# Kernel optimization log

Measured on AMD Instinct MI355X. Metric: run time of the kernel, lower is better.

## Reference

```python
import jax, jax.numpy as jnp
import numpy as np

NUM_HEADS = 16
ROPE_THETA = 10000.0


def _vision_rope_tables(seq_len, head_dim):
    # Llama4 vision ('mllama4') 2D rotary: x/y patch-grid positions,
    # interleaved (non-neox) complex pairs. Returns cos/sin [S, head_dim//2].
    idx = int(np.sqrt(seq_len))  # patches per side (24 for 336/14)
    pos = np.arange(seq_len)
    fx = (pos % idx + 1).astype(np.float32)
    fy = (pos // idx + 1).astype(np.float32)
    freq_dim = head_dim // 2
    rope_freq = 1.0 / ROPE_THETA ** (
        np.arange(0, freq_dim, 2)[: freq_dim // 2].astype(np.float32) / freq_dim
    )
    fx = np.repeat(fx[:, None] * rope_freq[None, :], 2, axis=-1)  # [S, freq_dim]
    fy = np.repeat(fy[:, None] * rope_freq[None, :], 2, axis=-1)
    freqs = np.concatenate([fx, fy], axis=-1)[:, ::2]  # [S, head_dim//2]
    return jnp.asarray(np.cos(freqs)), jnp.asarray(np.sin(freqs))


def _apply_rope(x, cos, sin):
    # x: [B, S, H, D]; even/odd interleaved pairs treated as complex numbers
    B, S, H, D = x.shape
    xr = x.reshape(B, S, H, D // 2, 2)
    x0, x1 = xr[..., 0], xr[..., 1]
    c = cos[None, :, None, :]
    s = sin[None, :, None, :]
    o0 = x0 * c - x1 * s
    o1 = x0 * s + x1 * c
    return jnp.stack([o0, o1], axis=-1).reshape(B, S, H, D)


def setup_inputs() -> dict:
    key = jax.random.key(0)
    ks = jax.random.split(key, 5)
    E = 1408
    B, S = 16, 576
    scale = 0.02
    return {
        "hidden_states": jax.random.normal(ks[0], (B, S, E), dtype=jnp.float32),
        "w_qkv": jax.random.normal(ks[1], (E, 3 * E), dtype=jnp.float32) * scale,
        "b_qkv": jax.random.normal(ks[2], (3 * E,), dtype=jnp.float32) * scale,
        "w_o": jax.random.normal(ks[3], (E, E), dtype=jnp.float32) * scale,
        "b_o": jax.random.normal(ks[4], (E,), dtype=jnp.float32) * scale,
    }


def reference(hidden_states, w_qkv, b_qkv, w_o, b_o):
    B, S, E = hidden_states.shape
    H = NUM_HEADS
    D = E // H
    scaling = D ** -0.5

    qkv = hidden_states @ w_qkv + b_qkv  # [B,S,3E]
    q, k, v = jnp.split(qkv, 3, axis=-1)
    q = q.reshape(B, S, H, D)
    k = k.reshape(B, S, H, D)
    v = v.reshape(B, S, H, D)

    cos, sin = _vision_rope_tables(S, D)
    q = _apply_rope(q, cos, sin)
    k = _apply_rope(k, cos, sin)

    q = q * scaling
    scores = jnp.einsum("bqhd,bkhd->bhqk", q, k)  # full bidirectional attention
    probs = jax.nn.softmax(scores, axis=-1)
    attn = jnp.einsum("bhqk,bkhd->bqhd", probs, v).reshape(B, S, E)

    return attn @ w_o + b_o
```

## Files before the change

### kernel.cpp

```cpp
#include <hip/hip_runtime.h>
#include <hip/hip_bf16.h>


typedef unsigned short UST;
typedef __attribute__((ext_vector_type(8))) __bf16 bf16x8;
typedef __attribute__((ext_vector_type(4))) float f32x4;
typedef __attribute__((ext_vector_type(8))) UST us8;
typedef __attribute__((ext_vector_type(4))) UST us4;

typedef __attribute__((address_space(3))) unsigned int lds_u32;
typedef const __attribute__((address_space(1))) unsigned int glob_u32;

static __device__ __forceinline__ float bf2f(UST u){
  unsigned int x = ((unsigned int)u) << 16;
  return __builtin_bit_cast(float, x);
}
static __device__ __forceinline__ UST f2bf(float f){
  unsigned int x = __builtin_bit_cast(unsigned int, f);
  x += 0x7fffu + ((x >> 16) & 1u);
  return (UST)(x >> 16);
}

__global__ void k_tables(float* __restrict__ cosT, float* __restrict__ sinT){
  int s = blockIdx.x;
  int d = threadIdx.x;
  if (d >= 88) return;
  int p = d >> 1;
  int tt = p % 22;
  double comp = (p < 22) ? (double)(s % 24 + 1) : (double)(s / 24 + 1);
  double a = comp * pow(10000.0, -(double)tt / 22.0);
  cosT[d*576 + s] = (float)cos(a);
  sinT[d*576 + s] = (float)sin(a);
}

__global__ void k_zero(UST* __restrict__ qa, UST* __restrict__ ka, UST* __restrict__ vt){
  int c = blockIdx.x*256 + threadIdx.x;
  int bh = c / 576, s = c - bh*576;
  us8 z = {0,0,0,0,0,0,0,0};
  *(us8*)(qa + ((size_t)bh*576 + s)*96 + 88) = z;
  *(us8*)(ka + ((size_t)bh*576 + s)*96 + 88) = z;
  *(us8*)(vt + (size_t)bh*55296 + 50688 + s*8) = z;
}

__global__ void k_cvt(const float* __restrict__ in, UST* __restrict__ out, int n4){
  int i = blockIdx.x * 256 + threadIdx.x;
  if (i >= n4) return;
  float4 v = ((const float4*)in)[i];
  us4 o; o[0]=f2bf(v.x); o[1]=f2bf(v.y); o[2]=f2bf(v.z); o[3]=f2bf(v.w);
  *(us4*)(out + 4*(size_t)i) = o;
}

__global__ void k_cvt_t(const float* __restrict__ W, UST* __restrict__ Bt, int K, int N){
  __shared__ __align__(16) UST tl[64][70];
  int kt = blockIdx.x, nt = blockIdx.y;
  int t = threadIdx.x;
  int k = t >> 2, u = t & 3;
  const float* src = W + (size_t)(kt*64 + k)*N + nt*64 + u*16;
#pragma unroll
  for (int i = 0; i < 4; ++i){
    float4 v = *(const float4*)(src + 4*i);
    UST* d = &tl[k][u*16 + 4*i];
    d[0]=f2bf(v.x); d[1]=f2bf(v.y); d[2]=f2bf(v.z); d[3]=f2bf(v.w);
  }
  __syncthreads();
  int n = t >> 2;
  UST* dst = Bt + (size_t)(nt*64 + n)*K + kt*64 + u*16;
#pragma unroll
  for (int i = 0; i < 2; ++i){
    us8 o;
#pragma unroll
    for (int j = 0; j < 8; ++j) o[j] = tl[u*16 + 8*i + j][n];
    *(us8*)(dst + 8*i) = o;
  }
}

template<int EPI>
__global__ __launch_bounds__(256, 2) void k_gemm(
    const UST* __restrict__ A, const UST* __restrict__ Bt,
    const float* __restrict__ bias, void* __restrict__ Cout,
    int M, int N, int K,
    UST* __restrict__ qa, UST* __restrict__ ka, UST* __restrict__ vt,
    const float* __restrict__ cosT, const float* __restrict__ sinT)
{
  __shared__ __align__(16) UST lA[2][128][64];
  __shared__ __align__(16) UST lB[2][128][64];
  const int t = threadIdx.x;
  const int bm = blockIdx.x, bn = blockIdx.y;
  const int wave = t >> 6, lane = t & 63;
  const int lm = lane & 15, g = lane >> 4;
  const int wr = (wave >> 1) << 6, wc = (wave & 1) << 6;
  const int lrow = lane >> 3;
  const int lcol = (((lane & 7) ^ lrow) << 3);
  const UST* Ag = A  + (size_t)(bm*128 + wave*32 + lrow)*K + lcol;
  const UST* Bg = Bt + (size_t)(bn*128 + wave*32 + lrow)*K + lcol;

  f32x4 zero = {0.f,0.f,0.f,0.f};
  f32x4 acc[4][4];
#pragma unroll
  for (int i=0;i<4;++i)
#pragma unroll
    for (int j=0;j<4;++j) acc[i][j] = zero;

  const int nkt = K >> 6;
  auto stage = [&](int kt, int buf){
#pragma unroll
    for (int c = 0; c < 4; ++c){
      __builtin_amdgcn_global_load_lds((glob_u32*)(Ag + (size_t)kt*64 + (size_t)(8*c)*K),
                                       (lds_u32*)(&lA[buf][wave*32 + 8*c][0]), 16, 0, 0);
      __builtin_amdgcn_global_load_lds((glob_u32*)(Bg + (size_t)kt*64 + (size_t)(8*c)*K),
                                       (lds_u32*)(&lB[buf][wave*32 + 8*c][0]), 16, 0, 0);
    }
  };

  stage(0, 0);
  __syncthreads();
  const int swz = (lm & 7) << 3;

  for (int kt = 0; kt < nkt; ++kt){
    const int cur = kt & 1;
    if (kt + 1 < nkt) stage(kt + 1, cur ^ 1);
#pragma unroll
    for (int ks = 0; ks < 2; ++ks){
      bf16x8 af[4], bfv[4];
      const int cb = (ks*32 + g*8) ^ swz;
#pragma unroll
      for (int mf = 0; mf < 4; ++mf)
        af[mf] = __builtin_bit_cast(bf16x8, *(const us8*)&lA[cur][wr + mf*16 + lm][cb]);
#pragma unroll
      for (int nf = 0; nf < 4; ++nf)
        bfv[nf] = __builtin_bit_cast(bf16x8, *(const us8*)&lB[cur][wc + nf*16 + lm][cb]);
#pragma unroll
      for (int mf = 0; mf < 4; ++mf)
#pragma unroll
        for (int nf = 0; nf < 4; ++nf)
          acc[mf][nf] = __builtin_amdgcn_mfma_f32_16x16x32_bf16(af[mf], bfv[nf], acc[mf][nf], 0, 0, 0);
    }
    __syncthreads();
  }

  if (EPI == 0){
#pragma unroll
    for (int nf = 0; nf < 4; ++nf){
      const int col = bn*128 + wc + nf*16 + lm;
      const float bv = bias[col];
#pragma unroll
      for (int mf = 0; mf < 4; ++mf){
        const size_t rb = (size_t)(bm*128 + wr + mf*16 + g*4);
#pragma unroll
        for (int r = 0; r < 4; ++r)
          ((float*)Cout)[(rb + r)*(size_t)N + col] = acc[mf][nf][r] + bv;
      }
    }
  } else {
    const int j = bn / 11;
    const int bnr = bn - j*11;
    if (j == 2){
#pragma unroll
      for (int nf = 0; nf < 4; ++nf){
        const int cv = bnr*128 + wc + nf*16 + lm;
        const float bv = bias[2816 + cv];
        const int h = cv / 88, d = cv - h*88;
#pragma unroll
        for (int mf = 0; mf < 4; ++mf){
          const int rb = bm*128 + wr + mf*16 + g*4;
          const int b2 = rb / 576, s = rb - b2*576;
          UST* dst = vt + ((size_t)((b2*16 + h)*96 + d))*576 + s;
          us4 pk;
#pragma unroll
          for (int r = 0; r < 4; ++r) pk[r] = f2bf(acc[mf][nf][r] + bv);
          *(us4*)dst = pk;
        }
      }
    } else {
      UST* outp = j ? ka : qa;
      const float sc = j ? 1.0f : 0.10660035817780521f;
      const bool even = (lm & 1) == 0;
#pragma unroll
      for (int nf = 0; nf < 4; ++nf){
        const int cv = bnr*128 + wc + nf*16 + lm;
        const float bv = bias[j*1408 + cv];
        const int h = cv / 88, d = cv - h*88;
        const float* cT = cosT + d*576;
        const float* sT = sinT + d*576;
#pragma unroll
        for (int mf = 0; mf < 4; ++mf){
          const int rb = bm*128 + wr + mf*16 + g*4;
          const int b2 = rb / 576, s = rb - b2*576;
          float4 c4 = *(const float4*)(cT + s);
          float4 s4 = *(const float4*)(sT + s);
          float cc[4] = {c4.x, c4.y, c4.z, c4.w};
          float ss[4] = {s4.x, s4.y, s4.z, s4.w};
          UST* dst = outp + ((size_t)(b2*16 + h)*576 + s)*96 + d;
#pragma unroll
          for (int r = 0; r < 4; ++r){
            float vs = acc[mf][nf][r] + bv;
            float vo = __shfl_xor(vs, 1, 64);
            float o = even ? (vs*cc[r] - vo*ss[r])
                           : (vo*ss[r] + vs*cc[r]);
            dst[(size_t)r*96] = f2bf(o * sc);
          }
        }
      }
    }
  }
}

__global__ __launch_bounds__(256, 2) void k_attn(
    const UST* __restrict__ qa, const UST* __restrict__ ka,
    const UST* __restrict__ vt, UST* __restrict__ outp)
{
  __shared__ __align__(16) UST lK[64][104];
  __shared__ __align__(16) UST lV[96][72];
  __shared__ __align__(16) UST lP[4][16][72];
  const int bh = blockIdx.x, qt = blockIdx.y;
  const int t = threadIdx.x, wave = t >> 6, lane = t & 63;
  const int lm = lane & 15, g = lane >> 4;
  const int h = bh & 15, b = bh >> 4;

  bf16x8 qf[3];
  {
    const UST* qp = qa + ((size_t)bh*576 + qt*64 + wave*16 + lm)*96 + g*8;
#pragma unroll
    for (int ks = 0; ks < 3; ++ks) qf[ks] = __builtin_bit_cast(bf16x8, *(const us8*)(qp + ks*32));
  }
  f32x4 zero = {0.f,0.f,0.f,0.f};
  f32x4 acc[6];
#pragma unroll
  for (int i = 0; i < 6; ++i) acc[i] = zero;
  float mrun[4], lrun[4];
#pragma unroll
  for (int r = 0; r < 4; ++r){ mrun[r] = -1e30f; lrun[r] = 0.f; }

  const UST* kbase = ka + (size_t)bh*576*96;
  const UST* vbase = vt + (size_t)bh*96*576;

  for (int kvt = 0; kvt < 9; ++kvt){
    {
      int r = t >> 2, u = t & 3;
      const UST* src = kbase + (size_t)(kvt*64 + r)*96 + u*24;
#pragma unroll
      for (int i = 0; i < 3; ++i)
        *(uint4*)&lK[r][u*24 + i*8] = *(const uint4*)(src + i*8);
    }
    if (t < 192){
      int d = t >> 1, hf = t & 1;
      const UST* src = vbase + (size_t)d*576 + kvt*64 + hf*32;
#pragma unroll
      for (int i = 0; i < 4; ++i)
        *(uint4*)&lV[d][hf*32 + i*8] = *(const uint4*)(src + i*8);
    }
    __syncthreads();

    f32x4 sc[4];
#pragma unroll
    for (int i = 0; i < 4; ++i) sc[i] = zero;
#pragma unroll
    for (int ks = 0; ks < 3; ++ks){
#pragma unroll
      for (int nf = 0; nf < 4; ++nf){
        bf16x8 kf = __builtin_bit_cast(bf16x8, *(const us8*)&lK[nf*16 + lm][ks*32 + g*8]);
        sc[nf] = __builtin_amdgcn_mfma_f32_16x16x32_bf16(qf[ks], kf, sc[nf], 0, 0, 0);
      }
    }
    float mx[4];
#pragma unroll
    for (int r = 0; r < 4; ++r)
      mx[r] = fmaxf(fmaxf(sc[0][r], sc[1][r]), fmaxf(sc[2][r], sc[3][r]));
#pragma unroll
    for (int m = 1; m <= 8; m <<= 1)
#pragma unroll
      for (int r = 0; r < 4; ++r) mx[r] = fmaxf(mx[r], __shfl_xor(mx[r], m, 64));
    float al[4];
#pragma unroll
    for (int r = 0; r < 4; ++r){
      float mnew = fmaxf(mrun[r], mx[r]);
      float corr = __expf(mrun[r] - mnew);
      mrun[r] = mnew;
      lrun[r] *= corr;
      float ls = 0.f;
#pragma unroll
      for (int nf = 0; nf < 4; ++nf){
        float p = __expf(sc[nf][r] - mnew);
        sc[nf][r] = p;
        ls += p;
      }
#pragma unroll
      for (int df = 0; df < 6; ++df) acc[df][r] *= corr;
      al[r] = ls;
    }
#pragma unroll
    for (int m = 1; m <= 8; m <<= 1)
#pragma unroll
      for (int r = 0; r < 4; ++r) al[r] += __shfl_xor(al[r], m, 64);
#pragma unroll
    for (int r = 0; r < 4; ++r) lrun[r] += al[r];

#pragma unroll
    for (int nf = 0; nf < 4; ++nf)
#pragma unroll
      for (int r = 0; r < 4; ++r)
        lP[wave][4*g + r][nf*16 + lm] = f2bf(sc[nf][r]);

    bf16x8 pa[2];
#pragma unroll
    for (int ks2 = 0; ks2 < 2; ++ks2)
      pa[ks2] = __builtin_bit_cast(bf16x8, *(const us8*)&lP[wave][lm][ks2*32 + g*8]);
#pragma unroll
    for (int ks2 = 0; ks2 < 2; ++ks2)
#pragma unroll
      for (int df = 0; df < 6; ++df){
        bf16x8 vf = __builtin_bit_cast(bf16x8, *(const us8*)&lV[df*16 + lm][ks2*32 + g*8]);
        acc[df] = __builtin_amdgcn_mfma_f32_16x16x32_bf16(pa[ks2], vf, acc[df], 0, 0, 0);
      }
    __syncthreads();
  }

  float inv[4];
#pragma unroll
  for (int r = 0; r < 4; ++r) inv[r] = 1.f / lrun[r];
  const size_t rowt = (size_t)b*576 + qt*64 + wave*16;
#pragma unroll
  for (int df = 0; df < 6; ++df){
    int d = df*16 + lm;
    if (d < 88){
#pragma unroll
      for (int r = 0; r < 4; ++r)
        outp[(rowt + 4*g + r)*1408 + h*88 + d] = f2bf(acc[df][r] * inv[r]);
    }
  }
}

extern "C" void kernel_launch(void* const* d_in, const int* in_sizes, int n_in,
                              void* d_out, int out_size, void* d_ws, size_t ws_size,
                              hipStream_t stream)
{
  (void)in_sizes; (void)n_in; (void)out_size; (void)ws_size;
  const float* hs   = (const float*)d_in[0];
  const float* wqkv = (const float*)d_in[1];
  const float* bqkv = (const float*)d_in[2];
  const float* wo   = (const float*)d_in[3];
  const float* bo   = (const float*)d_in[4];
  float* out = (float*)d_out;

  char* w = (char*)d_ws;
  UST* A_bf   = (UST*)(w);
  UST* Bt1    = (UST*)(w + 25952256);
  UST* Bt2    = (UST*)(w + 37847040);
  UST* qa     = (UST*)(w + 41811968);
  UST* ka     = (UST*)(w + 70123520);
  UST* vt     = (UST*)(w + 98435072);
  float* cosT = (float*)(w + 126746624);
  float* sinT = (float*)(w + 126949376);

  k_tables<<<576, 128, 0, stream>>>(cosT, sinT);
  k_zero<<<576, 256, 0, stream>>>(qa, ka, vt);
  k_cvt<<<12672, 256, 0, stream>>>(hs, A_bf, 3244032);
  k_cvt_t<<<dim3(22, 66), 256, 0, stream>>>(wqkv, Bt1, 1408, 4224);
  k_cvt_t<<<dim3(22, 22), 256, 0, stream>>>(wo, Bt2, 1408, 1408);
  k_gemm<3><<<dim3(72, 33), 256, 0, stream>>>(A_bf, Bt1, bqkv, nullptr, 9216, 4224, 1408,
                                              qa, ka, vt, cosT, sinT);
  k_attn<<<dim3(256, 9), 256, 0, stream>>>(qa, ka, vt, A_bf);
  k_gemm<0><<<dim3(72, 11), 256, 0, stream>>>(A_bf, Bt2, bo, out, 9216, 1408, 1408,
                                              nullptr, nullptr, nullptr, nullptr, nullptr);
}
```

Baseline: 330.0 us.

## Process two query tiles per attention block and pack RoPE epilogue stores

The attention kernel now handles two 64-row query tiles per block, so each loaded K/V tile in LDS serves 128 queries and block count drops from 9 to 5 per head. The last block handles one tile. Separately, the QKV GEMM RoPE epilogue has lane pairs each write two adjacent bf16 outputs as one 32-bit store, and loads only the two cos/sin values it needs. This trades more registers (two accumulator sets) and fewer blocks, with some load imbalance, for halved K/V global traffic and fewer narrow stores.

```diff
diff --git a/kernel.cpp b/kernel.cpp
--- a/kernel.cpp
+++ b/kernel.cpp
@@ -175,29 +175,38 @@
       UST* outp = j ? ka : qa;
       const float sc = j ? 1.0f : 0.10660035817780521f;
       const bool even = (lm & 1) == 0;
+      const int r0 = (lm & 1) * 2;
 #pragma unroll
       for (int nf = 0; nf < 4; ++nf){
         const int cv = bnr*128 + wc + nf*16 + lm;
         const float bv = bias[j*1408 + cv];
         const int h = cv / 88, d = cv - h*88;
+        const int de = d & ~1;
         const float* cT = cosT + d*576;
         const float* sT = sinT + d*576;
 #pragma unroll
         for (int mf = 0; mf < 4; ++mf){
           const int rb = bm*128 + wr + mf*16 + g*4;
           const int b2 = rb / 576, s = rb - b2*576;
-          float4 c4 = *(const float4*)(cT + s);
-          float4 s4 = *(const float4*)(sT + s);
-          float cc[4] = {c4.x, c4.y, c4.z, c4.w};
-          float ss[4] = {s4.x, s4.y, s4.z, s4.w};
-          UST* dst = outp + ((size_t)(b2*16 + h)*576 + s)*96 + d;
+          float2 c2 = *(const float2*)(cT + s + r0);
+          float2 s2 = *(const float2*)(sT + s + r0);
+          UST* dstE = outp + ((size_t)(b2*16 + h)*576 + s)*96 + de;
+          float vs[4], vo[4];
 #pragma unroll
           for (int r = 0; r < 4; ++r){
-            float vs = acc[mf][nf][r] + bv;
-            float vo = __shfl_xor(vs, 1, 64);
-            float o = even ? (vs*cc[r] - vo*ss[r])
-                           : (vo*ss[r] + vs*cc[r]);
-            dst[(size_t)r*96] = f2bf(o * sc);
+            vs[r] = acc[mf][nf][r] + bv;
+            vo[r] = __shfl_xor(vs[r], 1, 64);
+          }
+          float cc[2] = {c2.x, c2.y}, ss[2] = {s2.x, s2.y};
+#pragma unroll
+          for (int rr = 0; rr < 2; ++rr){
+            const int r = r0 + rr;
+            float x0 = even ? vs[r] : vo[r];
+            float x1 = even ? vo[r] : vs[r];
+            float o0 = (x0*cc[rr] - x1*ss[rr])*sc;
+            float o1 = (x0*ss[rr] + x1*cc[rr])*sc;
+            unsigned int pk = (unsigned int)f2bf(o0) | ((unsigned int)f2bf(o1) << 16);
+            *(unsigned int*)(dstE + (size_t)r*96) = pk;
           }
         }
       }
@@ -212,35 +221,40 @@
   __shared__ __align__(16) UST lK[64][104];
   __shared__ __align__(16) UST lV[96][72];
   __shared__ __align__(16) UST lP[4][16][72];
-  const int bh = blockIdx.x, qt = blockIdx.y;
+  const int bh = blockIdx.x, qt2 = blockIdx.y;
+  const int nset = (qt2 == 4) ? 1 : 2;
   const int t = threadIdx.x, wave = t >> 6, lane = t & 63;
   const int lm = lane & 15, g = lane >> 4;
   const int h = bh & 15, b = bh >> 4;
 
-  bf16x8 qf[3];
-  {
-    const UST* qp = qa + ((size_t)bh*576 + qt*64 + wave*16 + lm)*96 + g*8;
-#pragma unroll
-    for (int ks = 0; ks < 3; ++ks) qf[ks] = __builtin_bit_cast(bf16x8, *(const us8*)(qp + ks*32));
-  }
+  bf16x8 qf[2][3];
   f32x4 zero = {0.f,0.f,0.f,0.f};
-  f32x4 acc[6];
-#pragma unroll
-  for (int i = 0; i < 6; ++i) acc[i] = zero;
-  float mrun[4], lrun[4];
-#pragma unroll
-  for (int r = 0; r < 4; ++r){ mrun[r] = -1e30f; lrun[r] = 0.f; }
+  f32x4 acc[2][6];
+  float mrun[2][4], lrun[2][4];
+#pragma unroll
+  for (int u = 0; u < 2; ++u){
+    if (u < nset){
+      const UST* qp = qa + ((size_t)bh*576 + qt2*128 + u*64 + wave*16 + lm)*96 + g*8;
+#pragma unroll
+      for (int ks = 0; ks < 3; ++ks)
+        qf[u][ks] = __builtin_bit_cast(bf16x8, *(const us8*)(qp + ks*32));
+    }
+#pragma unroll
+    for (int i = 0; i < 6; ++i) acc[u][i] = zero;
+#pragma unroll
+    for (int r = 0; r < 4; ++r){ mrun[u][r] = -1e30f; lrun[u][r] = 0.f; }
+  }
 
   const UST* kbase = ka + (size_t)bh*576*96;
   const UST* vbase = vt + (size_t)bh*96*576;
 
   for (int kvt = 0; kvt < 9; ++kvt){
     {
-      int r = t >> 2, u = t & 3;
-      const UST* src = kbase + (size_t)(kvt*64 + r)*96 + u*24;
+      int r = t >> 2, u4 = t & 3;
+      const UST* src = kbase + (size_t)(kvt*64 + r)*96 + u4*24;
 #pragma unroll
       for (int i = 0; i < 3; ++i)
-        *(uint4*)&lK[r][u*24 + i*8] = *(const uint4*)(src + i*8);
+        *(uint4*)&lK[r][u4*24 + i*8] = *(const uint4*)(src + i*8);
     }
     if (t < 192){
       int d = t >> 1, hf = t & 1;
@@ -251,81 +265,89 @@
     }
     __syncthreads();
 
-    f32x4 sc[4];
-#pragma unroll
-    for (int i = 0; i < 4; ++i) sc[i] = zero;
-#pragma unroll
-    for (int ks = 0; ks < 3; ++ks){
-#pragma unroll
-      for (int nf = 0; nf < 4; ++nf){
-        bf16x8 kf = __builtin_bit_cast(bf16x8, *(const us8*)&lK[nf*16 + lm][ks*32 + g*8]);
-        sc[nf] = __builtin_amdgcn_mfma_f32_16x16x32_bf16(qf[ks], kf, sc[nf], 0, 0, 0);
-      }
-    }
-    float mx[4];
-#pragma unroll
-    for (int r = 0; r < 4; ++r)
-      mx[r] = fmaxf(fmaxf(sc[0][r], sc[1][r]), fmaxf(sc[2][r], sc[3][r]));
-#pragma unroll
-    for (int m = 1; m <= 8; m <<= 1)
-#pragma unroll
-      for (int r = 0; r < 4; ++r) mx[r] = fmaxf(mx[r], __shfl_xor(mx[r], m, 64));
-    float al[4];
-#pragma unroll
-    for (int r = 0; r < 4; ++r){
-      float mnew = fmaxf(mrun[r], mx[r]);
-      float corr = __expf(mrun[r] - mnew);
-      mrun[r] = mnew;
-      lrun[r] *= corr;
-      float ls = 0.f;
-#pragma unroll
-      for (int nf = 0; nf < 4; ++nf){
-        float p = __expf(sc[nf][r] - mnew);
-        sc[nf][r] = p;
-        ls += p;
-      }
-#pragma unroll
-      for (int df = 0; df < 6; ++df) acc[df][r] *= corr;
-      al[r] = ls;
-    }
-#pragma unroll
-    for (int m = 1; m <= 8; m <<= 1)
-#pragma unroll
-      for (int r = 0; r < 4; ++r) al[r] += __shfl_xor(al[r], m, 64);
-#pragma unroll
-    for (int r = 0; r < 4; ++r) lrun[r] += al[r];
-
-#pragma unroll
-    for (int nf = 0; nf < 4; ++nf)
+#pragma unroll
+    for (int u = 0; u < 2; ++u){
+      if (u >= nset) continue;
+      f32x4 sc[4];
+#pragma unroll
+      for (int i = 0; i < 4; ++i) sc[i] = zero;
+#pragma unroll
+      for (int ks = 0; ks < 3; ++ks){
+#pragma unroll
+        for (int nf = 0; nf < 4; ++nf){
+          bf16x8 kf = __builtin_bit_cast(bf16x8, *(const us8*)&lK[nf*16 + lm][ks*32 + g*8]);
+          sc[nf] = __builtin_amdgcn_mfma_f32_16x16x32_bf16(qf[u][ks], kf, sc[nf], 0, 0, 0);
+        }
+      }
+      float mx[4];
 #pragma unroll
       for (int r = 0; r < 4; ++r)
-        lP[wave][4*g + r][nf*16 + lm] = f2bf(sc[nf][r]);
-
-    bf16x8 pa[2];
-#pragma unroll
-    for (int ks2 = 0; ks2 < 2; ++ks2)
-      pa[ks2] = __builtin_bit_cast(bf16x8, *(const us8*)&lP[wave][lm][ks2*32 + g*8]);
-#pragma unroll
-    for (int ks2 = 0; ks2 < 2; ++ks2)
-#pragma unroll
-      for (int df = 0; df < 6; ++df){
-        bf16x8 vf = __builtin_bit_cast(bf16x8, *(const us8*)&lV[df*16 + lm][ks2*32 + g*8]);
-        acc[df] = __builtin_amdgcn_mfma_f32_16x16x32_bf16(pa[ks2], vf, acc[df], 0, 0, 0);
-      }
+        mx[r] = fmaxf(fmaxf(sc[0][r], sc[1][r]), fmaxf(sc[2][r], sc[3][r]));
+#pragma unroll
+      for (int m = 1; m <= 8; m <<= 1)
+#pragma unroll
+        for (int r = 0; r < 4; ++r) mx[r] = fmaxf(mx[r], __shfl_xor(mx[r], m, 64));
+      float al[4];
+#pragma unroll
+      for (int r = 0; r < 4; ++r){
+        float mnew = fmaxf(mrun[u][r], mx[r]);
+        float corr = __expf(mrun[u][r] - mnew);
+        mrun[u][r] = mnew;
+        lrun[u][r] *= corr;
+        float ls = 0.f;
+#pragma unroll
+        for (int nf = 0; nf < 4; ++nf){
+          float p = __expf(sc[nf][r] - mnew);
+          sc[nf][r] = p;
+          ls += p;
+        }
+#pragma unroll
+        for (int df = 0; df < 6; ++df) acc[u][df][r] *= corr;
+        al[r] = ls;
+      }
+#pragma unroll
+      for (int m = 1; m <= 8; m <<= 1)
+#pragma unroll
+        for (int r = 0; r < 4; ++r) al[r] += __shfl_xor(al[r], m, 64);
+#pragma unroll
+      for (int r = 0; r < 4; ++r) lrun[u][r] += al[r];
+
+#pragma unroll
+      for (int nf = 0; nf < 4; ++nf)
+#pragma unroll
+        for (int r = 0; r < 4; ++r)
+          lP[wave][4*g + r][nf*16 + lm] = f2bf(sc[nf][r]);
+
+      bf16x8 pa[2];
+#pragma unroll
+      for (int ks2 = 0; ks2 < 2; ++ks2)
+        pa[ks2] = __builtin_bit_cast(bf16x8, *(const us8*)&lP[wave][lm][ks2*32 + g*8]);
+#pragma unroll
+      for (int ks2 = 0; ks2 < 2; ++ks2)
+#pragma unroll
+        for (int df = 0; df < 6; ++df){
+          bf16x8 vf = __builtin_bit_cast(bf16x8, *(const us8*)&lV[df*16 + lm][ks2*32 + g*8]);
+          acc[u][df] = __builtin_amdgcn_mfma_f32_16x16x32_bf16(pa[ks2], vf, acc[u][df], 0, 0, 0);
+        }
+    }
     __syncthreads();
   }
 
-  float inv[4];
-#pragma unroll
-  for (int r = 0; r < 4; ++r) inv[r] = 1.f / lrun[r];
-  const size_t rowt = (size_t)b*576 + qt*64 + wave*16;
-#pragma unroll
-  for (int df = 0; df < 6; ++df){
-    int d = df*16 + lm;
-    if (d < 88){
-#pragma unroll
-      for (int r = 0; r < 4; ++r)
-        outp[(rowt + 4*g + r)*1408 + h*88 + d] = f2bf(acc[df][r] * inv[r]);
+#pragma unroll
+  for (int u = 0; u < 2; ++u){
+    if (u >= nset) continue;
+    float inv[4];
+#pragma unroll
+    for (int r = 0; r < 4; ++r) inv[r] = 1.f / lrun[u][r];
+    const size_t rowt = (size_t)b*576 + qt2*128 + u*64 + wave*16;
+#pragma unroll
+    for (int df = 0; df < 6; ++df){
+      int d = df*16 + lm;
+      if (d < 88){
+#pragma unroll
+        for (int r = 0; r < 4; ++r)
+          outp[(rowt + 4*g + r)*1408 + h*88 + d] = f2bf(acc[u][df][r] * inv[r]);
+      }
     }
   }
 }
@@ -359,7 +381,7 @@
   k_cvt_t<<<dim3(22, 22), 256, 0, stream>>>(wo, Bt2, 1408, 1408);
   k_gemm<3><<<dim3(72, 33), 256, 0, stream>>>(A_bf, Bt1, bqkv, nullptr, 9216, 4224, 1408,
                                               qa, ka, vt, cosT, sinT);
-  k_attn<<<dim3(256, 9), 256, 0, stream>>>(qa, ka, vt, A_bf);
+  k_attn<<<dim3(256, 5), 256, 0, stream>>>(qa, ka, vt, A_bf);
   k_gemm<0><<<dim3(72, 11), 256, 0, stream>>>(A_bf, Bt2, bo, out, 9216, 1408, 1408,
                                               nullptr, nullptr, nullptr, nullptr, nullptr);
 }
```

After: 357.5 us. +8.3%, slower.

## Load K/V MFMA fragments directly from global memory instead of staging through LDS

Applied to the files above, without the earlier changes.

The attention kernel drops the shared-memory K and V tiles and the block-wide barriers. Each wave now loads its K and V MFMA operand fragments straight from global memory, relying on L2/L1 to serve the reuse across the four waves. The grid is transposed so the 9 query tiles of one (batch, head) are launched next to each other, which should improve cache hits on K/V. s_setprio is raised around the MFMA sections. The cost is more global and cache traffic with uncoalesced 16-byte loads per lane, plus higher register pressure from holding 24 fragments.

```diff
diff --git a/kernel.cpp b/kernel.cpp
--- a/kernel.cpp
+++ b/kernel.cpp
@@ -209,10 +209,8 @@
     const UST* __restrict__ qa, const UST* __restrict__ ka,
     const UST* __restrict__ vt, UST* __restrict__ outp)
 {
-  __shared__ __align__(16) UST lK[64][104];
-  __shared__ __align__(16) UST lV[96][72];
   __shared__ __align__(16) UST lP[4][16][72];
-  const int bh = blockIdx.x, qt = blockIdx.y;
+  const int qt = blockIdx.x, bh = blockIdx.y;
   const int t = threadIdx.x, wave = t >> 6, lane = t & 63;
   const int lm = lane & 15, g = lane >> 4;
   const int h = bh & 15, b = bh >> 4;
@@ -231,37 +229,37 @@
 #pragma unroll
   for (int r = 0; r < 4; ++r){ mrun[r] = -1e30f; lrun[r] = 0.f; }
 
-  const UST* kbase = ka + (size_t)bh*576*96;
-  const UST* vbase = vt + (size_t)bh*96*576;
+  const UST* kb = ka + ((size_t)bh*576 + lm)*96 + g*8;
+  const UST* vb = vt + ((size_t)bh*96 + lm)*576 + g*8;
 
   for (int kvt = 0; kvt < 9; ++kvt){
-    {
-      int r = t >> 2, u = t & 3;
-      const UST* src = kbase + (size_t)(kvt*64 + r)*96 + u*24;
-#pragma unroll
-      for (int i = 0; i < 3; ++i)
-        *(uint4*)&lK[r][u*24 + i*8] = *(const uint4*)(src + i*8);
-    }
-    if (t < 192){
-      int d = t >> 1, hf = t & 1;
-      const UST* src = vbase + (size_t)d*576 + kvt*64 + hf*32;
-#pragma unroll
-      for (int i = 0; i < 4; ++i)
-        *(uint4*)&lV[d][hf*32 + i*8] = *(const uint4*)(src + i*8);
-    }
-    __syncthreads();
+    bf16x8 kf[3][4];
+#pragma unroll
+    for (int nf = 0; nf < 4; ++nf)
+#pragma unroll
+      for (int ks = 0; ks < 3; ++ks)
+        kf[ks][nf] = __builtin_bit_cast(bf16x8,
+          *(const us8*)(kb + (size_t)(kvt*64 + nf*16)*96 + ks*32));
 
     f32x4 sc[4];
 #pragma unroll
     for (int i = 0; i < 4; ++i) sc[i] = zero;
-#pragma unroll
-    for (int ks = 0; ks < 3; ++ks){
-#pragma unroll
-      for (int nf = 0; nf < 4; ++nf){
-        bf16x8 kf = __builtin_bit_cast(bf16x8, *(const us8*)&lK[nf*16 + lm][ks*32 + g*8]);
-        sc[nf] = __builtin_amdgcn_mfma_f32_16x16x32_bf16(qf[ks], kf, sc[nf], 0, 0, 0);
-      }
-    }
+    __builtin_amdgcn_s_setprio(1);
+#pragma unroll
+    for (int ks = 0; ks < 3; ++ks)
+#pragma unroll
+      for (int nf = 0; nf < 4; ++nf)
+        sc[nf] = __builtin_amdgcn_mfma_f32_16x16x32_bf16(qf[ks], kf[ks][nf], sc[nf], 0, 0, 0);
+    __builtin_amdgcn_s_setprio(0);
+
+    bf16x8 vf[2][6];
+#pragma unroll
+    for (int df = 0; df < 6; ++df)
+#pragma unroll
+      for (int ks2 = 0; ks2 < 2; ++ks2)
+        vf[ks2][df] = __builtin_bit_cast(bf16x8,
+          *(const us8*)(vb + (size_t)(df*16)*576 + kvt*64 + ks2*32));
+
     float mx[4];
 #pragma unroll
     for (int r = 0; r < 4; ++r)
@@ -305,14 +303,13 @@
 #pragma unroll
     for (int ks2 = 0; ks2 < 2; ++ks2)
       pa[ks2] = __builtin_bit_cast(bf16x8, *(const us8*)&lP[wave][lm][ks2*32 + g*8]);
+    __builtin_amdgcn_s_setprio(1);
 #pragma unroll
     for (int ks2 = 0; ks2 < 2; ++ks2)
 #pragma unroll
-      for (int df = 0; df < 6; ++df){
-        bf16x8 vf = __builtin_bit_cast(bf16x8, *(const us8*)&lV[df*16 + lm][ks2*32 + g*8]);
-        acc[df] = __builtin_amdgcn_mfma_f32_16x16x32_bf16(pa[ks2], vf, acc[df], 0, 0, 0);
-      }
-    __syncthreads();
+      for (int df = 0; df < 6; ++df)
+        acc[df] = __builtin_amdgcn_mfma_f32_16x16x32_bf16(pa[ks2], vf[ks2][df], acc[df], 0, 0, 0);
+    __builtin_amdgcn_s_setprio(0);
   }
 
   float inv[4];
@@ -359,7 +356,7 @@
   k_cvt_t<<<dim3(22, 22), 256, 0, stream>>>(wo, Bt2, 1408, 1408);
   k_gemm<3><<<dim3(72, 33), 256, 0, stream>>>(A_bf, Bt1, bqkv, nullptr, 9216, 4224, 1408,
                                               qa, ka, vt, cosT, sinT);
-  k_attn<<<dim3(256, 9), 256, 0, stream>>>(qa, ka, vt, A_bf);
+  k_attn<<<dim3(9, 256), 256, 0, stream>>>(qa, ka, vt, A_bf);
   k_gemm<0><<<dim3(72, 11), 256, 0, stream>>>(A_bf, Bt2, bo, out, 9216, 1408, 1408,
                                               nullptr, nullptr, nullptr, nullptr, nullptr);
 }
```

Result: slower. 401.4 us (+21.6%).
